# Optimization experiments

Hardware: AMD Instinct MI355X
Metric: run time of the kernel (lower is better)

The kernel has to match this reference:

```python
import jax, jax.numpy as jnp
import numpy as np

N, D_IN, D_H, D_ATT, C_CLUST, N_CLS = 10000, 1024, 512, 256, 10, 4


def setup_inputs() -> dict:
    key = jax.random.key(0)
    ks = jax.random.split(key, 20)
    s = 0.02
    return {
        "x": jax.random.normal(ks[0], (N, D_IN), dtype=jnp.float32),
        "cluster_id": jax.random.randint(ks[1], (N,), 0, C_CLUST, dtype=jnp.int64),
        # per-cluster phi: Linear(1024->512) + ReLU + Linear(512->512) + ReLU
        "W1": s * jax.random.normal(ks[2], (C_CLUST, D_IN, D_H), dtype=jnp.float32),
        "b1": jnp.zeros((C_CLUST, D_H), dtype=jnp.float32),
        "W2": s * jax.random.normal(ks[3], (C_CLUST, D_H, D_H), dtype=jnp.float32),
        "b2": jnp.zeros((C_CLUST, D_H), dtype=jnp.float32),
        # attention_net fc: Linear(512->512)+ReLU
        "Wfc": s * jax.random.normal(ks[4], (D_H, D_H), dtype=jnp.float32),
        "bfc": jnp.zeros((D_H,), dtype=jnp.float32),
        # Attn_Net_Gated
        "Wa": s * jax.random.normal(ks[5], (D_H, D_ATT), dtype=jnp.float32),
        "ba": jnp.zeros((D_ATT,), dtype=jnp.float32),
        "Wb": s * jax.random.normal(ks[6], (D_H, D_ATT), dtype=jnp.float32),
        "bb": jnp.zeros((D_ATT,), dtype=jnp.float32),
        "Wc": s * jax.random.normal(ks[7], (D_ATT, 1), dtype=jnp.float32),
        "bc": jnp.zeros((1,), dtype=jnp.float32),
        # rho: Linear(512->256)+ReLU
        "Wr": s * jax.random.normal(ks[8], (D_H, D_ATT), dtype=jnp.float32),
        "br": jnp.zeros((D_ATT,), dtype=jnp.float32),
        # classifier: Linear(256->4)
        "Wcls": s * jax.random.normal(ks[9], (D_ATT, N_CLS), dtype=jnp.float32),
        "bcls": jnp.zeros((N_CLS,), dtype=jnp.float32),
    }


def reference(x, cluster_id, W1, b1, W2, b2, Wfc, bfc, Wa, ba, Wb, bb, Wc, bc, Wr, br, Wcls, bcls):
    C = W1.shape[0]
    # dense dispatch: apply every cluster's phi, then masked-mean per cluster
    # (ReLU is per-point elementwise, so masked mean == mean over members)
    h1 = jax.nn.relu(jnp.einsum('nd,cdh->cnh', x, W1) + b1[:, None, :])   # [C,N,512]
    h2 = jax.nn.relu(jnp.einsum('cnh,chk->cnk', h1, W2) + b2[:, None, :]) # [C,N,512]
    mask = (cluster_id[None, :] == jnp.arange(C)[:, None]).astype(h2.dtype)  # [C,N]
    counts = jnp.maximum(mask.sum(axis=1), 1.0)                           # [C]
    pooled = jnp.einsum('cnk,cn->ck', h2, mask) / counts[:, None]         # [C,512]
    # attention_net: fc + gated attention
    h = jax.nn.relu(pooled @ Wfc + bfc)                                   # [C,512]
    gate = jnp.tanh(h @ Wa + ba) * jax.nn.sigmoid(h @ Wb + bb)            # [C,256]
    A = (gate @ Wc + bc)                                                  # [C,1]
    A = jax.nn.softmax(A.T, axis=1)                                       # [1,C]
    h_path = A @ h                                                        # [1,512]
    hr = jax.nn.relu(h_path @ Wr + br)                                    # [1,256]
    logits = (hr[0] @ Wcls + bcls)[None, :]                               # [1,4]
    Y_prob = jax.nn.softmax(logits, axis=1)
    Y_hat = jnp.argmax(logits, axis=1)[:, None]
    return logits, Y_prob, Y_hat
```

## Files before the change

### kernel.cpp

```cpp
#include <hip/hip_runtime.h>
#include <math.h>

#define DIN 1024
#define DH 512
#define DATT 256
#define CNUM 10
#define NCLS 4
#define NH 64
#define NSC 40

typedef __attribute__((ext_vector_type(8))) short bf16x8;
typedef __attribute__((ext_vector_type(4))) float f32x4;
typedef unsigned short ushort_t;
typedef unsigned int uint_t;

__device__ inline ushort_t f2bf(float f) {
    uint_t u = __float_as_uint(f);
    u += 0x7FFF + ((u >> 16) & 1);
    return (ushort_t)(u >> 16);
}

__device__ inline void gl_lds16(const void* g, void* l) {
    __builtin_amdgcn_global_load_lds(
        (const __attribute__((address_space(1))) unsigned int*)g,
        (__attribute__((address_space(3))) unsigned int*)l, 16, 0, 0);
}


__global__ __launch_bounds__(256) void k_pre1(
    const float* __restrict__ x, const int* __restrict__ cid, int n,
    const float* __restrict__ bc,
    const float* __restrict__ W1, const float* __restrict__ W2,
    ushort_t* __restrict__ xb, ushort_t* __restrict__ W1t, ushort_t* __restrict__ W2t,
    int nxb, int nw,
    int* __restrict__ counts_part, float* __restrict__ pooled, float* __restrict__ a_logit)
{
    int bid = blockIdx.x;
    int t = threadIdx.x;

    if (bid < nxb) {
        int row = bid * 2 + (t >> 7);
        if (row >= n) return;
        int col = (t & 127) * 8;
        const float* src = x + (size_t)row * DIN + col;
        float4 v0 = *(const float4*)(src);
        float4 v1 = *(const float4*)(src + 4);
        ushort_t* dst = xb + (size_t)row * DIN + col;
        *(ushort4*)dst = make_ushort4(f2bf(v0.x), f2bf(v0.y), f2bf(v0.z), f2bf(v0.w));
        *(ushort4*)(dst + 4) = make_ushort4(f2bf(v1.x), f2bf(v1.y), f2bf(v1.z), f2bf(v1.w));
        return;
    }
    bid -= nxb;

    if (bid < nw) {
        __shared__ float tile[64][65];
        int z = bid >> 7;
        int kx = (bid & 127) >> 3;
        int ny = bid & 7;
        const float* src; ushort_t* dst; int K;
        if (z < CNUM) { K = DIN; src = W1 + (size_t)z * K * DH; dst = W1t + (size_t)z * DH * K; }
        else          { K = DH;  src = W2 + (size_t)(z - CNUM) * K * DH; dst = W2t + (size_t)(z - CNUM) * DH * K; }
        int k0 = kx * 64;
        if (k0 >= K) return;
        int n0 = ny * 64;
        int rr = t >> 4;
        int cc = (t & 15) * 4;
        #pragma unroll
        for (int i = 0; i < 4; i++) {
            int row = rr + 16 * i;
            float4 v = *(const float4*)(src + (size_t)(k0 + row) * DH + n0 + cc);
            tile[row][cc + 0] = v.x; tile[row][cc + 1] = v.y;
            tile[row][cc + 2] = v.z; tile[row][cc + 3] = v.w;
        }
        __syncthreads();
        #pragma unroll
        for (int i = 0; i < 4; i++) {
            int nrow = rr + 16 * i;
            ushort4 o = make_ushort4(f2bf(tile[cc + 0][nrow]), f2bf(tile[cc + 1][nrow]),
                                     f2bf(tile[cc + 2][nrow]), f2bf(tile[cc + 3][nrow]));
            *(ushort4*)(dst + (size_t)(n0 + nrow) * K + k0 + cc) = o;
        }
        return;
    }
    bid -= nw;

    if (bid < NH) {
        __shared__ int h[CNUM];
        int lane = t & 63;
        if (t < CNUM) h[t] = 0;
        __syncthreads();
        for (int i = bid * 256 + t; i < n; i += NH * 256) {
            int c = cid[i];
            #pragma unroll
            for (int cc = 0; cc < CNUM; cc++) {
                unsigned long long mask = __ballot(c == cc);
                if (mask == 0ull) continue;
                if (lane == (__ffsll(mask) - 1)) atomicAdd(&h[cc], __popcll(mask));
            }
        }
        __syncthreads();
        if (t < CNUM) counts_part[bid * 16 + t] = h[t];
        return;
    }

    for (int i = t; i < CNUM * DH; i += 256) pooled[i] = 0.f;
    if (t < CNUM) a_logit[t] = bc[0];
}


__global__ void k_pre2(
    const int* __restrict__ counts_part,
    int* __restrict__ counts, int* __restrict__ offsets, int* __restrict__ tile_off,
    int* __restrict__ cursors)
{
    int t = threadIdx.x;
    if (t < CNUM) {
        int s = 0;
        #pragma unroll 8
        for (int b = 0; b < NH; b++) s += counts_part[b * 16 + t];
        counts[t] = s;
    }
    __syncthreads();
    if (t == 0) {
        int a = 0, tt = 0;
        for (int c = 0; c < CNUM; c++) {
            offsets[c] = a; tile_off[c] = tt; cursors[c] = a;
            a += counts[c]; tt += (counts[c] + 127) >> 7;
        }
        offsets[CNUM] = a; tile_off[CNUM] = tt;
    }
}


__global__ __launch_bounds__(256) void k_pre3(
    const int* __restrict__ cid, int n,
    int* __restrict__ cursors, int* __restrict__ bucket)
{
    int t = threadIdx.x;
    int lane = t & 63;
    for (int i = blockIdx.x * 256 + t; i < n; i += NSC * 256) {
        int c = cid[i];
        #pragma unroll
        for (int cc = 0; cc < CNUM; cc++) {
            unsigned long long mask = __ballot(c == cc);
            if (mask == 0ull) continue;
            int leader = __ffsll(mask) - 1;
            int basep = 0;
            if (lane == leader) basep = atomicAdd(&cursors[cc], __popcll(mask));
            basep = __shfl(basep, leader, 64);
            if (c == cc) {
                int rank = __popcll(mask & ((1ull << lane) - 1ull));
                bucket[basep + rank] = i;
            }
        }
    }
}


__device__ inline void gemm_tile(
    const ushort_t* aSrc0, const ushort_t* aSrc1,
    const ushort_t* bSrc0, const ushort_t* bSrc1, int Kd,
    f32x4 acc[4][4], ushort_t As[128][32], ushort_t Bs[128][32])
{
    int t = threadIdx.x;
    int lane = t & 63;
    int w = t >> 6, wr = w >> 1, wc = w & 1;
    int m = lane & 15, quad = lane >> 4;

    int r0 = t >> 2;
    int kc = (t & 3) * 8;

    ushort_t* aDst0 = &As[r0][kc];
    ushort_t* aDst1 = &As[64 + r0][kc];
    ushort_t* bDst0 = &Bs[r0][kc];
    ushort_t* bDst1 = &Bs[64 + r0][kc];

    const ushort_t* aF = &As[64 * wr + m][quad * 8];
    const ushort_t* bF = &Bs[64 * wc + m][quad * 8];

    for (int k0 = 0; k0 < Kd; k0 += 32) {
        __syncthreads();
        gl_lds16(aSrc0 + k0, aDst0);
        gl_lds16(aSrc1 + k0, aDst1);
        gl_lds16(bSrc0 + k0, bDst0);
        gl_lds16(bSrc1 + k0, bDst1);
        __syncthreads();
        bf16x8 a[4], b[4];
        #pragma unroll
        for (int mf = 0; mf < 4; mf++) a[mf] = *(const bf16x8*)(aF + mf * 16 * 32);
        #pragma unroll
        for (int nf = 0; nf < 4; nf++) b[nf] = *(const bf16x8*)(bF + nf * 16 * 32);
        #pragma unroll
        for (int mf = 0; mf < 4; mf++)
            #pragma unroll
            for (int nf = 0; nf < 4; nf++)
                acc[mf][nf] = __builtin_amdgcn_mfma_f32_16x16x32_bf16(a[mf], b[nf], acc[mf][nf], 0, 0, 0);
    }
}

__global__ __launch_bounds__(256, 1) void k_mfma1(
    const ushort_t* __restrict__ xb, const ushort_t* __restrict__ W1t,
    const float* __restrict__ b1, const int* __restrict__ bucket,
    const int* __restrict__ offsets, const int* __restrict__ counts,
    const int* __restrict__ tile_off,
    ushort_t* __restrict__ H1)
{
    __shared__ ushort_t As[128][32];
    __shared__ ushort_t Bs[128][32];
    int tx = blockIdx.x;
    if (tx >= tile_off[CNUM]) return;
    int c = 0;
    while (tx >= tile_off[c + 1]) c++;
    int m0 = (tx - tile_off[c]) * 128;
    int base = offsets[c], cnt = counts[c];
    int tile_n = blockIdx.y * 128;

    int t = threadIdx.x;
    int r0 = t >> 2;
    int kc = (t & 3) * 8;
    int ra0 = m0 + r0;      if (ra0 > cnt - 1) ra0 = cnt - 1; if (ra0 < 0) ra0 = 0;
    int ra1 = m0 + 64 + r0; if (ra1 > cnt - 1) ra1 = cnt - 1; if (ra1 < 0) ra1 = 0;
    const ushort_t* aSrc0 = xb + (size_t)bucket[base + ra0] * DIN + kc;
    const ushort_t* aSrc1 = xb + (size_t)bucket[base + ra1] * DIN + kc;
    const ushort_t* bSrc0 = W1t + ((size_t)c * DH + tile_n + r0) * DIN + kc;
    const ushort_t* bSrc1 = W1t + ((size_t)c * DH + tile_n + 64 + r0) * DIN + kc;

    f32x4 acc[4][4] = {};
    gemm_tile(aSrc0, aSrc1, bSrc0, bSrc1, DIN, acc, As, Bs);

    int lane = t & 63;
    int w = t >> 6, wr = w >> 1, wc = w & 1;
    int m = lane & 15, quad = lane >> 4;
    int col0 = tile_n + 64 * wc;
    #pragma unroll
    for (int nf = 0; nf < 4; nf++) {
        int col = col0 + 16 * nf + m;
        float bv = b1[c * DH + col];
        #pragma unroll
        for (int mf = 0; mf < 4; mf++) {
            int rowb = m0 + 64 * wr + 16 * mf + quad * 4;
            #pragma unroll
            for (int r = 0; r < 4; r++) {
                int row = rowb + r;
                if (row < cnt)
                    H1[(size_t)(base + row) * DH + col] = f2bf(fmaxf(acc[mf][nf][r] + bv, 0.f));
            }
        }
    }
}

__global__ __launch_bounds__(256, 1) void k_mfma2(
    const ushort_t* __restrict__ H1, const ushort_t* __restrict__ W2t,
    const float* __restrict__ b2,
    const int* __restrict__ offsets, const int* __restrict__ counts,
    const int* __restrict__ tile_off,
    float* __restrict__ pooled)
{
    __shared__ ushort_t As[128][32];
    __shared__ ushort_t Bs[128][32];
    int tx = blockIdx.x;
    if (tx >= tile_off[CNUM]) return;
    int c = 0;
    while (tx >= tile_off[c + 1]) c++;
    int m0 = (tx - tile_off[c]) * 128;
    int base = offsets[c], cnt = counts[c];
    int tile_n = blockIdx.y * 128;

    int t = threadIdx.x;
    int r0 = t >> 2;
    int kc = (t & 3) * 8;
    int ra0 = m0 + r0;      if (ra0 > cnt - 1) ra0 = cnt - 1; if (ra0 < 0) ra0 = 0;
    int ra1 = m0 + 64 + r0; if (ra1 > cnt - 1) ra1 = cnt - 1; if (ra1 < 0) ra1 = 0;
    const ushort_t* aSrc0 = H1 + (size_t)(base + ra0) * DH + kc;
    const ushort_t* aSrc1 = H1 + (size_t)(base + ra1) * DH + kc;
    const ushort_t* bSrc0 = W2t + ((size_t)c * DH + tile_n + r0) * DH + kc;
    const ushort_t* bSrc1 = W2t + ((size_t)c * DH + tile_n + 64 + r0) * DH + kc;

    f32x4 acc[4][4] = {};
    gemm_tile(aSrc0, aSrc1, bSrc0, bSrc1, DH, acc, As, Bs);

    int lane = t & 63;
    int w = t >> 6, wr = w >> 1, wc = w & 1;
    int m = lane & 15, quad = lane >> 4;
    int col0 = tile_n + 64 * wc;
    #pragma unroll
    for (int nf = 0; nf < 4; nf++) {
        int col = col0 + 16 * nf + m;
        float bv = b2[c * DH + col];
        float s = 0.f;
        #pragma unroll
        for (int mf = 0; mf < 4; mf++) {
            int rowb = m0 + 64 * wr + 16 * mf + quad * 4;
            #pragma unroll
            for (int r = 0; r < 4; r++) {
                int row = rowb + r;
                if (row < cnt) s += fmaxf(acc[mf][nf][r] + bv, 0.f);
            }
        }
        s += __shfl_xor(s, 16);
        s += __shfl_xor(s, 32);
        if (quad == 0) atomicAdd(&pooled[c * DH + col], s);
    }
}


#define MT 64
#define NT 128
#define KT 32

__global__ __launch_bounds__(256) void k_gemm1(
    const float* __restrict__ x, const float* __restrict__ W1, const float* __restrict__ b1,
    const int* __restrict__ bucket, const int* __restrict__ offsets, const int* __restrict__ counts,
    float* __restrict__ H1)
{
    int c = blockIdx.z;
    int cnt = counts[c];
    int m0 = blockIdx.x * MT;
    if (m0 >= cnt) return;
    int rows = min(MT, cnt - m0);
    int n0 = blockIdx.y * NT;
    int base = offsets[c];

    __shared__ float As[KT][MT + 4];
    __shared__ float Bs[KT][NT];

    int t = threadIdx.x;
    int tr = t >> 4;
    int tc = t & 15;
    int lr = t >> 2;
    int lk = (t & 3) * 8;
    const float* xrow = nullptr;
    if (lr < rows) xrow = x + (size_t)bucket[base + m0 + lr] * DIN;

    float acc[4][8];
    #pragma unroll
    for (int i = 0; i < 4; i++)
        #pragma unroll
        for (int j = 0; j < 8; j++) acc[i][j] = 0.f;
// ... 108 lines not shown
        #pragma unroll
        for (int k = 0; k < KT; k++) {
            float4 av  = *(const float4*)&As[k][4 * tr];
            float4 bv0 = *(const float4*)&Bs[k][4 * tc];
            float4 bv1 = *(const float4*)&Bs[k][64 + 4 * tc];
            float a[4] = {av.x, av.y, av.z, av.w};
            float b[8] = {bv0.x, bv0.y, bv0.z, bv0.w, bv1.x, bv1.y, bv1.z, bv1.w};
            #pragma unroll
            for (int i = 0; i < 4; i++)
                #pragma unroll
                for (int j = 0; j < 8; j++)
                    acc[i][j] = fmaf(a[i], b[j], acc[i][j]);
        }
    }

    __syncthreads();
    #pragma unroll
    for (int j = 0; j < 8; j++) {
        int cidx = (j < 4) ? (4 * tc + j) : (64 + 4 * tc + (j - 4));
        float bias = b2[c * DH + n0 + cidx];
        float s = 0.f;
        #pragma unroll
        for (int i = 0; i < 4; i++) {
            if (4 * tr + i < rows) s += fmaxf(acc[i][j] + bias, 0.f);
        }
        red[tr][cidx] = s;
    }
    __syncthreads();
    if (t < NT) {
        float s = 0.f;
        #pragma unroll
        for (int r = 0; r < 16; r++) s += red[r][t];
        atomicAdd(&pooled[c * DH + n0 + t], s);
    }
}


__global__ __launch_bounds__(256) void k_fc2(
    const float* __restrict__ pooled, const int* __restrict__ counts,
    const float* __restrict__ Wfc, const float* __restrict__ bfc,
    float* __restrict__ hfc)
{
    int c = blockIdx.x;
    int c0 = blockIdx.y * 64;
    __shared__ float ps[DH];
    __shared__ float red[4][64];
    int t = threadIdx.x;
    float cnt = fmaxf((float)counts[c], 1.f);
    ps[t] = pooled[c * DH + t] / cnt;
    ps[t + 256] = pooled[c * DH + t + 256] / cnt;
    __syncthreads();
    int col = c0 + (t & 63);
    int ks = t >> 6;
    float acc = 0.f;
    #pragma unroll 8
    for (int k = ks * 128; k < ks * 128 + 128; k++)
        acc = fmaf(ps[k], Wfc[(size_t)k * DH + col], acc);
    red[ks][t & 63] = acc;
    __syncthreads();
    if (t < 64) {
        float v = red[0][t] + red[1][t] + red[2][t] + red[3][t] + bfc[c0 + t];
        hfc[c * DH + c0 + t] = fmaxf(v, 0.f);
    }
}

__global__ __launch_bounds__(256) void k_gate2(
    const float* __restrict__ hfc,
    const float* __restrict__ Wa, const float* __restrict__ ba,
    const float* __restrict__ Wb, const float* __restrict__ bb,
    const float* __restrict__ Wc,
    float* __restrict__ a_logit)
{
    int c = blockIdx.x;
    int d0 = blockIdx.y * 64;
    __shared__ float hf[DH];
    __shared__ float ra[4][64], rb[4][64];
    int t = threadIdx.x;
    hf[t] = hfc[c * DH + t];
    hf[t + 256] = hfc[c * DH + t + 256];
    __syncthreads();
    int d = d0 + (t & 63);
    int ks = t >> 6;
    float ga = 0.f, gb = 0.f;
    #pragma unroll 8
    for (int k = ks * 128; k < ks * 128 + 128; k++) {
        float h = hf[k];
        ga = fmaf(h, Wa[(size_t)k * DATT + d], ga);
        gb = fmaf(h, Wb[(size_t)k * DATT + d], gb);
    }
    ra[ks][t & 63] = ga;
    rb[ks][t & 63] = gb;
    __syncthreads();
    if (t < 64) {
        float sa = ra[0][t] + ra[1][t] + ra[2][t] + ra[3][t] + ba[d0 + t];
        float sb = rb[0][t] + rb[1][t] + rb[2][t] + rb[3][t] + bb[d0 + t];
        float g = tanhf(sa) * (1.f / (1.f + expf(-sb)));
        float p = g * Wc[d0 + t];
        #pragma unroll
        for (int off = 32; off >= 1; off >>= 1) p += __shfl_down(p, off, 64);
        if (t == 0) atomicAdd(&a_logit[c], p);
    }
}

__global__ __launch_bounds__(1024) void k_final(
    const float* __restrict__ hfc, const float* __restrict__ a_logit,
    const float* __restrict__ Wr, const float* __restrict__ br,
    const float* __restrict__ Wcls, const float* __restrict__ bcls,
    float* __restrict__ out)
{
    int t = threadIdx.x;
    __shared__ float hp[DH];
    __shared__ float r1[4][DATT];
    __shared__ float hr[DATT];
    __shared__ float wred[4][NCLS];

    float al[CNUM];
    float m = -1e30f;
    #pragma unroll
    for (int c = 0; c < CNUM; c++) { al[c] = a_logit[c]; m = fmaxf(m, al[c]); }
    float s = 0.f;
    #pragma unroll
    for (int c = 0; c < CNUM; c++) { al[c] = expf(al[c] - m); s += al[c]; }
    float inv = 1.f / s;

    if (t < DH) {
        float v = 0.f;
        #pragma unroll
        for (int c = 0; c < CNUM; c++) v = fmaf(al[c] * inv, hfc[c * DH + t], v);
        hp[t] = v;
    }
    __syncthreads();

    int d = t & 255;
    int ks = t >> 8;
    float acc = 0.f;
    #pragma unroll 8
    for (int k = ks * 128; k < ks * 128 + 128; k++)
        acc = fmaf(hp[k], Wr[(size_t)k * DATT + d], acc);
    r1[ks][d] = acc;
    __syncthreads();
    if (t < DATT)
        hr[t] = fmaxf(r1[0][t] + r1[1][t] + r1[2][t] + r1[3][t] + br[t], 0.f);
    __syncthreads();

    if (t < 256) {
        float h = hr[t];
        #pragma unroll
        for (int cls = 0; cls < NCLS; cls++) {
            float p = h * Wcls[(size_t)t * NCLS + cls];
            #pragma unroll
            for (int off = 32; off >= 1; off >>= 1) p += __shfl_down(p, off, 64);
            if ((t & 63) == 0) wred[t >> 6][cls] = p;
        }
    }
    __syncthreads();
    if (t == 0) {
        float lg[NCLS];
        #pragma unroll
        for (int cls = 0; cls < NCLS; cls++)
            lg[cls] = bcls[cls] + wred[0][cls] + wred[1][cls] + wred[2][cls] + wred[3][cls];
        float mm = lg[0];
        #pragma unroll
        for (int i = 1; i < NCLS; i++) mm = fmaxf(mm, lg[i]);
        float ss = 0.f, pr[NCLS];
        #pragma unroll
        for (int i = 0; i < NCLS; i++) { pr[i] = expf(lg[i] - mm); ss += pr[i]; }
        int am = 0; float best = lg[0];
        #pragma unroll
        for (int i = 1; i < NCLS; i++) if (lg[i] > best) { best = lg[i]; am = i; }
        #pragma unroll
        for (int i = 0; i < NCLS; i++) out[i] = lg[i];
        #pragma unroll
        for (int i = 0; i < NCLS; i++) out[4 + i] = pr[i] / ss;
        out[8] = (float)am;
    }
}


extern "C" void kernel_launch(void* const* d_in, const int* in_sizes, int n_in,
                              void* d_out, int out_size, void* d_ws, size_t ws_size,
                              hipStream_t stream) {
    (void)n_in; (void)out_size;
    const float* x    = (const float*)d_in[0];
    const int*   cid  = (const int*)d_in[1];
    const float* W1   = (const float*)d_in[2];
    const float* b1   = (const float*)d_in[3];
    const float* W2   = (const float*)d_in[4];
    const float* b2   = (const float*)d_in[5];
    const float* Wfc  = (const float*)d_in[6];
    const float* bfc  = (const float*)d_in[7];
    const float* Wa   = (const float*)d_in[8];
    const float* ba   = (const float*)d_in[9];
    const float* Wb   = (const float*)d_in[10];
    const float* bb   = (const float*)d_in[11];
    const float* Wc   = (const float*)d_in[12];
    const float* bc   = (const float*)d_in[13];
    const float* Wr   = (const float*)d_in[14];
    const float* br   = (const float*)d_in[15];
    const float* Wcls = (const float*)d_in[16];
    const float* bcls = (const float*)d_in[17];
    float* out = (float*)d_out;
    float* ws  = (float*)d_ws;

    int n = in_sizes[1];

    float* pooled     = ws + 0;
    int*   counts     = (int*)(ws + 5120);
    int*   offsets    = (int*)(ws + 5136);
    int*   tile_off   = (int*)(ws + 5152);
    float* a_logit    = ws + 5168;
    int*   cursors    = (int*)(ws + 5184);
    float* hfc        = ws + 5200;
    int*   counts_part= (int*)(ws + 10320);
    int*   bucket     = (int*)(ws + 11344);

    size_t big0 = (((size_t)(11344 + n) * 4) + 255) & ~(size_t)255;
    size_t w1t_bytes = (size_t)CNUM * DH * DIN * 2;
    size_t w2t_bytes = (size_t)CNUM * DH * DH * 2;
    size_t h1_bytes  = (size_t)n * DH * 2;
    size_t xb_bytes  = (size_t)n * DIN * 2;
    size_t need = big0 + w1t_bytes + w2t_bytes + h1_bytes + xb_bytes;

    ushort_t* W1t = (ushort_t*)((char*)d_ws + big0);
    ushort_t* W2t = (ushort_t*)((char*)d_ws + big0 + w1t_bytes);
    ushort_t* H1  = (ushort_t*)((char*)d_ws + big0 + w1t_bytes + w2t_bytes);
    ushort_t* xb  = (ushort_t*)((char*)d_ws + big0 + w1t_bytes + w2t_bytes + h1_bytes);

    int fast = (ws_size >= need) ? 1 : 0;
    int nxb = fast ? (n + 1) / 2 : 0;
    int nw  = fast ? 128 * 2 * CNUM : 0;
    int pre1_blocks = nxb + nw + NH + 1;

    k_pre1<<<pre1_blocks, 256, 0, stream>>>(
        x, cid, n, bc, W1, W2, xb, W1t, W2t, nxb, nw,
        counts_part, pooled, a_logit);
    k_pre2<<<1, 64, 0, stream>>>(counts_part, counts, offsets, tile_off, cursors);
    k_pre3<<<NSC, 256, 0, stream>>>(cid, n, cursors, bucket);

    if (fast) {
        int maxt = n / 128 + CNUM;
        k_mfma1<<<dim3(maxt, DH / 128), 256, 0, stream>>>(xb, W1t, b1, bucket, offsets, counts, tile_off, H1);
        k_mfma2<<<dim3(maxt, DH / 128), 256, 0, stream>>>(H1, W2t, b2, offsets, counts, tile_off, pooled);
    } else {
        float* H1f = ws + ((11344 + n + 31) & ~31);
        dim3 gg((n + MT - 1) / MT, DH / NT, CNUM);
        k_gemm1<<<gg, 256, 0, stream>>>(x, W1, b1, bucket, offsets, counts, H1f);
        k_gemm2<<<gg, 256, 0, stream>>>(H1f, W2, b2, offsets, counts, pooled);
    }

    k_fc2<<<dim3(CNUM, 8), 256, 0, stream>>>(pooled, counts, Wfc, bfc, hfc);
    k_gate2<<<dim3(CNUM, 4), 256, 0, stream>>>(hfc, Wa, ba, Wb, bb, Wc, a_logit);
    k_final<<<1, 1024, 0, stream>>>(hfc, a_logit, Wr, br, Wcls, bcls, out);
}
```

Measured before the change: 245.4 us.

## Fuse pre2/pre3 into scatter kernel and merge tail kernels with spin-wait flags

Merges the count-prefix kernel into the scatter kernel: every block recomputes the offsets and scatters with per-cluster relative cursors. The three tail kernels (fc, gate, final) become one 121-block launch that orders its phases with atomic done-counters and spin-waits. The GEMM grids are also transposed so blocks that share an M-tile launch next to each other. The aim is to cut launch overhead and improve L2 reuse of the gathered A rows, at the cost of spin-wait deadlock risk if the dependent blocks are not co-resident.

After: 258.4 us. +5.3%, slower.

```diff
diff --git a/kernel.cpp b/kernel.cpp
--- a/kernel.cpp
+++ b/kernel.cpp
@@ -26,6 +26,10 @@
         (__attribute__((address_space(3))) unsigned int*)l, 16, 0, 0);
 }
 
+__device__ inline float agent_load(const float* p) {
+    return __hip_atomic_load(p, __ATOMIC_RELAXED, __HIP_MEMORY_SCOPE_AGENT);
+}
+
 
 __global__ __launch_bounds__(256) void k_pre1(
     const float* __restrict__ x, const int* __restrict__ cid, int n,
@@ -33,7 +37,8 @@
     const float* __restrict__ W1, const float* __restrict__ W2,
     ushort_t* __restrict__ xb, ushort_t* __restrict__ W1t, ushort_t* __restrict__ W2t,
     int nxb, int nw,
-    int* __restrict__ counts_part, float* __restrict__ pooled, float* __restrict__ a_logit)
+    int* __restrict__ counts_part, float* __restrict__ pooled, float* __restrict__ a_logit,
+    int* __restrict__ scat_pos, int* __restrict__ fc_done, int* __restrict__ gate_done)
 {
     int bid = blockIdx.x;
     int t = threadIdx.x;
@@ -105,38 +110,39 @@
 
     for (int i = t; i < CNUM * DH; i += 256) pooled[i] = 0.f;
     if (t < CNUM) a_logit[t] = bc[0];
-}
-
-
-__global__ void k_pre2(
-    const int* __restrict__ counts_part,
+    if (t < CNUM) scat_pos[t] = 0;
+    if (t < CNUM) fc_done[t] = 0;
+    if (t == 0) gate_done[0] = 0;
+}
+
+
+__global__ __launch_bounds__(256) void k_scat(
+    const int* __restrict__ cid, int n, const int* __restrict__ counts_part,
     int* __restrict__ counts, int* __restrict__ offsets, int* __restrict__ tile_off,
-    int* __restrict__ cursors)
+    int* __restrict__ scat_pos, int* __restrict__ bucket)
 {
+    __shared__ int cnts[CNUM], off[CNUM];
     int t = threadIdx.x;
     if (t < CNUM) {
         int s = 0;
         #pragma unroll 8
         for (int b = 0; b < NH; b++) s += counts_part[b * 16 + t];
-        counts[t] = s;
+        cnts[t] = s;
     }
     __syncthreads();
     if (t == 0) {
-        int a = 0, tt = 0;
-        for (int c = 0; c < CNUM; c++) {
-            offsets[c] = a; tile_off[c] = tt; cursors[c] = a;
-            a += counts[c]; tt += (counts[c] + 127) >> 7;
-        }
-        offsets[CNUM] = a; tile_off[CNUM] = tt;
-    }
-}
-
-
-__global__ __launch_bounds__(256) void k_pre3(
-    const int* __restrict__ cid, int n,
-    int* __restrict__ cursors, int* __restrict__ bucket)
-{
-    int t = threadIdx.x;
+        int a = 0;
+        for (int c = 0; c < CNUM; c++) { off[c] = a; a += cnts[c]; }
+        if (blockIdx.x == 0) {
+            int aa = 0, tt = 0;
+            for (int c = 0; c < CNUM; c++) {
+                offsets[c] = aa; tile_off[c] = tt; counts[c] = cnts[c];
+                aa += cnts[c]; tt += (cnts[c] + 127) >> 7;
+            }
+            offsets[CNUM] = aa; tile_off[CNUM] = tt;
+        }
+    }
+    __syncthreads();
     int lane = t & 63;
     for (int i = blockIdx.x * 256 + t; i < n; i += NSC * 256) {
         int c = cid[i];
@@ -146,11 +152,11 @@
             if (mask == 0ull) continue;
             int leader = __ffsll(mask) - 1;
             int basep = 0;
-            if (lane == leader) basep = atomicAdd(&cursors[cc], __popcll(mask));
+            if (lane == leader) basep = atomicAdd(&scat_pos[cc], __popcll(mask));
             basep = __shfl(basep, leader, 64);
             if (c == cc) {
                 int rank = __popcll(mask & ((1ull << lane) - 1ull));
-                bucket[basep + rank] = i;
+                bucket[off[cc] + basep + rank] = i;
             }
         }
     }
@@ -207,13 +213,13 @@
 {
     __shared__ ushort_t As[128][32];
     __shared__ ushort_t Bs[128][32];
-    int tx = blockIdx.x;
+    int tx = blockIdx.y;
     if (tx >= tile_off[CNUM]) return;
     int c = 0;
     while (tx >= tile_off[c + 1]) c++;
     int m0 = (tx - tile_off[c]) * 128;
     int base = offsets[c], cnt = counts[c];
-    int tile_n = blockIdx.y * 128;
+    int tile_n = blockIdx.x * 128;
 
     int t = threadIdx.x;
     int r0 = t >> 2;
@@ -258,13 +264,13 @@
 {
     __shared__ ushort_t As[128][32];
     __shared__ ushort_t Bs[128][32];
-    int tx = blockIdx.x;
+    int tx = blockIdx.y;
     if (tx >= tile_off[CNUM]) return;
     int c = 0;
     while (tx >= tile_off[c + 1]) c++;
     int m0 = (tx - tile_off[c]) * 128;
     int base = offsets[c], cnt = counts[c];
-    int tile_n = blockIdx.y * 128;
+    int tile_n = blockIdx.x * 128;
 
     int t = threadIdx.x;
     int r0 = t >> 2;
@@ -300,6 +306,145 @@
         s += __shfl_xor(s, 16);
         s += __shfl_xor(s, 32);
         if (quad == 0) atomicAdd(&pooled[c * DH + col], s);
+    }
+}
+
+
+__global__ __launch_bounds__(256) void k_tail(
+    const float* __restrict__ pooled, const int* __restrict__ counts,
+    const float* __restrict__ Wfc, const float* __restrict__ bfc,
+    const float* __restrict__ Wa, const float* __restrict__ ba,
+    const float* __restrict__ Wb, const float* __restrict__ bb,
+    const float* __restrict__ Wc,
+    const float* __restrict__ Wr, const float* __restrict__ br,
+    const float* __restrict__ Wcls, const float* __restrict__ bcls,
+    float* __restrict__ hfc, float* __restrict__ a_logit,
+    int* __restrict__ fc_done, int* __restrict__ gate_done,
+    float* __restrict__ out)
+{
+    __shared__ float sh0[DH];
+    __shared__ float red4[4][DATT];
+    __shared__ float hr[DATT];
+    __shared__ float wred[4][NCLS];
+
+    int bid = blockIdx.x, t = threadIdx.x;
+
+    if (bid < 80) {
+        int c = bid >> 3;
+        int c0 = (bid & 7) * 64;
+        float cnt = fmaxf((float)counts[c], 1.f);
+        sh0[t] = pooled[c * DH + t] / cnt;
+        sh0[t + 256] = pooled[c * DH + t + 256] / cnt;
+        __syncthreads();
+        int col = c0 + (t & 63);
+        int ks = t >> 6;
+        float acc = 0.f;
+        #pragma unroll 8
+        for (int k = ks * 128; k < ks * 128 + 128; k++)
+            acc = fmaf(sh0[k], Wfc[(size_t)k * DH + col], acc);
+        red4[ks][t & 63] = acc;
+        __syncthreads();
+        if (t < 64) {
+            float v = red4[0][t] + red4[1][t] + red4[2][t] + red4[3][t] + bfc[c0 + t];
+            hfc[c * DH + c0 + t] = fmaxf(v, 0.f);
+        }
+        __threadfence();
+        __syncthreads();
+        if (t == 0) atomicAdd(&fc_done[c], 1);
+        return;
+    }
+
+    if (bid < 120) {
+        int b = bid - 80;
+        int c = b >> 2;
+        int d0 = (b & 3) * 64;
+        if (t == 0) { while (atomicAdd(&fc_done[c], 0) < 8) {} }
+        __syncthreads();
+        __threadfence();
+        sh0[t] = agent_load(&hfc[c * DH + t]);
+        sh0[t + 256] = agent_load(&hfc[c * DH + t + 256]);
+        __syncthreads();
+        int d = d0 + (t & 63);
+        int ks = t >> 6;
+        float ga = 0.f, gb = 0.f;
+        #pragma unroll 8
+        for (int k = ks * 128; k < ks * 128 + 128; k++) {
+            float h = sh0[k];
+            ga = fmaf(h, Wa[(size_t)k * DATT + d], ga);
+            gb = fmaf(h, Wb[(size_t)k * DATT + d], gb);
+        }
+        red4[ks][t & 63] = ga;
+        red4[ks][(t & 63) + 64] = gb;
+        __syncthreads();
+        if (t < 64) {
+            float sa = red4[0][t] + red4[1][t] + red4[2][t] + red4[3][t] + ba[d0 + t];
+            float sb = red4[0][t + 64] + red4[1][t + 64] + red4[2][t + 64] + red4[3][t + 64] + bb[d0 + t];
+            float g = tanhf(sa) * (1.f / (1.f + expf(-sb)));
+            float p = g * Wc[d0 + t];
+            #pragma unroll
+            for (int off = 32; off >= 1; off >>= 1) p += __shfl_down(p, off, 64);
+            if (t == 0) atomicAdd(&a_logit[c], p);
+        }
+        __threadfence();
+        __syncthreads();
+        if (t == 0) atomicAdd(gate_done, 1);
+        return;
+    }
+
+    if (t == 0) { while (atomicAdd(gate_done, 0) < 40) {} }
+    __syncthreads();
+    __threadfence();
+
+    float al[CNUM];
+    float m = -1e30f;
+    #pragma unroll
+    for (int c = 0; c < CNUM; c++) { al[c] = agent_load(&a_logit[c]); m = fmaxf(m, al[c]); }
+    float s = 0.f;
+    #pragma unroll
+    for (int c = 0; c < CNUM; c++) { al[c] = expf(al[c] - m); s += al[c]; }
+    float inv = 1.f / s;
+
+    for (int kk = t; kk < DH; kk += 256) {
+        float v = 0.f;
+        #pragma unroll
+        for (int c = 0; c < CNUM; c++) v = fmaf(al[c] * inv, agent_load(&hfc[c * DH + kk]), v);
+        sh0[kk] = v;
+    }
+    __syncthreads();
+
+    float acc = br[t];
+    for (int k = 0; k < DH; k++) acc = fmaf(sh0[k], Wr[(size_t)k * DATT + t], acc);
+    hr[t] = fmaxf(acc, 0.f);
+    __syncthreads();
+
+    float h = hr[t];
+    #pragma unroll
+    for (int cls = 0; cls < NCLS; cls++) {
+        float p = h * Wcls[(size_t)t * NCLS + cls];
+        #pragma unroll
+        for (int off = 32; off >= 1; off >>= 1) p += __shfl_down(p, off, 64);
+        if ((t & 63) == 0) wred[t >> 6][cls] = p;
+    }
+    __syncthreads();
+    if (t == 0) {
+        float lg[NCLS];
+        #pragma unroll
+        for (int cls = 0; cls < NCLS; cls++)
+            lg[cls] = bcls[cls] + wred[0][cls] + wred[1][cls] + wred[2][cls] + wred[3][cls];
+        float mm = lg[0];
+        #pragma unroll
+        for (int i = 1; i < NCLS; i++) mm = fmaxf(mm, lg[i]);
+        float ss = 0.f, pr[NCLS];
+        #pragma unroll
+        for (int i = 0; i < NCLS; i++) { pr[i] = expf(lg[i] - mm); ss += pr[i]; }
+        int am = 0; float best = lg[0];
+        #pragma unroll
+        for (int i = 1; i < NCLS; i++) if (lg[i] > best) { best = lg[i]; am = i; }
+        #pragma unroll
+        for (int i = 0; i < NCLS; i++) out[i] = lg[i];
+        #pragma unroll
+        for (int i = 0; i < NCLS; i++) out[4 + i] = pr[i] / ss;
+        out[8] = (float)am;
     }
 }
 
@@ -478,147 +623,6 @@
         #pragma unroll
         for (int r = 0; r < 16; r++) s += red[r][t];
         atomicAdd(&pooled[c * DH + n0 + t], s);
-    }
-}
-
-
-__global__ __launch_bounds__(256) void k_fc2(
-    const float* __restrict__ pooled, const int* __restrict__ counts,
-    const float* __restrict__ Wfc, const float* __restrict__ bfc,
-    float* __restrict__ hfc)
-{
-    int c = blockIdx.x;
-    int c0 = blockIdx.y * 64;
-    __shared__ float ps[DH];
-    __shared__ float red[4][64];
-    int t = threadIdx.x;
-    float cnt = fmaxf((float)counts[c], 1.f);
-    ps[t] = pooled[c * DH + t] / cnt;
-    ps[t + 256] = pooled[c * DH + t + 256] / cnt;
-    __syncthreads();
-    int col = c0 + (t & 63);
-    int ks = t >> 6;
-    float acc = 0.f;
-    #pragma unroll 8
-    for (int k = ks * 128; k < ks * 128 + 128; k++)
-        acc = fmaf(ps[k], Wfc[(size_t)k * DH + col], acc);
-    red[ks][t & 63] = acc;
-    __syncthreads();
-    if (t < 64) {
-        float v = red[0][t] + red[1][t] + red[2][t] + red[3][t] + bfc[c0 + t];
-        hfc[c * DH + c0 + t] = fmaxf(v, 0.f);
-    }
-}
-
-__global__ __launch_bounds__(256) void k_gate2(
-    const float* __restrict__ hfc,
-    const float* __restrict__ Wa, const float* __restrict__ ba,
-    const float* __restrict__ Wb, const float* __restrict__ bb,
-    const float* __restrict__ Wc,
-    float* __restrict__ a_logit)
-{
-    int c = blockIdx.x;
-    int d0 = blockIdx.y * 64;
-    __shared__ float hf[DH];
-    __shared__ float ra[4][64], rb[4][64];
-    int t = threadIdx.x;
-    hf[t] = hfc[c * DH + t];
-    hf[t + 256] = hfc[c * DH + t + 256];
-    __syncthreads();
-    int d = d0 + (t & 63);
-    int ks = t >> 6;
-    float ga = 0.f, gb = 0.f;
-    #pragma unroll 8
-    for (int k = ks * 128; k < ks * 128 + 128; k++) {
-        float h = hf[k];
-        ga = fmaf(h, Wa[(size_t)k * DATT + d], ga);
-        gb = fmaf(h, Wb[(size_t)k * DATT + d], gb);
-    }
-    ra[ks][t & 63] = ga;
-    rb[ks][t & 63] = gb;
-    __syncthreads();
-    if (t < 64) {
-        float sa = ra[0][t] + ra[1][t] + ra[2][t] + ra[3][t] + ba[d0 + t];
-        float sb = rb[0][t] + rb[1][t] + rb[2][t] + rb[3][t] + bb[d0 + t];
-        float g = tanhf(sa) * (1.f / (1.f + expf(-sb)));
-        float p = g * Wc[d0 + t];
-        #pragma unroll
-        for (int off = 32; off >= 1; off >>= 1) p += __shfl_down(p, off, 64);
-        if (t == 0) atomicAdd(&a_logit[c], p);
-    }
-}
-
-__global__ __launch_bounds__(1024) void k_final(
-    const float* __restrict__ hfc, const float* __restrict__ a_logit,
-    const float* __restrict__ Wr, const float* __restrict__ br,
-    const float* __restrict__ Wcls, const float* __restrict__ bcls,
-    float* __restrict__ out)
-{
-    int t = threadIdx.x;
-    __shared__ float hp[DH];
-    __shared__ float r1[4][DATT];
-    __shared__ float hr[DATT];
-    __shared__ float wred[4][NCLS];
-
-    float al[CNUM];
-    float m = -1e30f;
-    #pragma unroll
-    for (int c = 0; c < CNUM; c++) { al[c] = a_logit[c]; m = fmaxf(m, al[c]); }
-    float s = 0.f;
-    #pragma unroll
-    for (int c = 0; c < CNUM; c++) { al[c] = expf(al[c] - m); s += al[c]; }
-    float inv = 1.f / s;
-
-    if (t < DH) {
-        float v = 0.f;
-        #pragma unroll
-        for (int c = 0; c < CNUM; c++) v = fmaf(al[c] * inv, hfc[c * DH + t], v);
-        hp[t] = v;
-    }
-    __syncthreads();
-
-    int d = t & 255;
-    int ks = t >> 8;
-    float acc = 0.f;
-    #pragma unroll 8
-    for (int k = ks * 128; k < ks * 128 + 128; k++)
-        acc = fmaf(hp[k], Wr[(size_t)k * DATT + d], acc);
-    r1[ks][d] = acc;
-    __syncthreads();
-    if (t < DATT)
-        hr[t] = fmaxf(r1[0][t] + r1[1][t] + r1[2][t] + r1[3][t] + br[t], 0.f);
-    __syncthreads();
-
-    if (t < 256) {
-        float h = hr[t];
-        #pragma unroll
-        for (int cls = 0; cls < NCLS; cls++) {
-            float p = h * Wcls[(size_t)t * NCLS + cls];
-            #pragma unroll
-            for (int off = 32; off >= 1; off >>= 1) p += __shfl_down(p, off, 64);
-            if ((t & 63) == 0) wred[t >> 6][cls] = p;
-        }
-    }
-    __syncthreads();
-    if (t == 0) {
-        float lg[NCLS];
-        #pragma unroll
-        for (int cls = 0; cls < NCLS; cls++)
-            lg[cls] = bcls[cls] + wred[0][cls] + wred[1][cls] + wred[2][cls] + wred[3][cls];
-        float mm = lg[0];
-        #pragma unroll
-        for (int i = 1; i < NCLS; i++) mm = fmaxf(mm, lg[i]);
-        float ss = 0.f, pr[NCLS];
-        #pragma unroll
-        for (int i = 0; i < NCLS; i++) { pr[i] = expf(lg[i] - mm); ss += pr[i]; }
-        int am = 0; float best = lg[0];
-        #pragma unroll
-        for (int i = 1; i < NCLS; i++) if (lg[i] > best) { best = lg[i]; am = i; }
-        #pragma unroll
-        for (int i = 0; i < NCLS; i++) out[i] = lg[i];
-        #pragma unroll
-        for (int i = 0; i < NCLS; i++) out[4 + i] = pr[i] / ss;
-        out[8] = (float)am;
     }
 }
 
@@ -655,12 +659,14 @@
     int*   offsets    = (int*)(ws + 5136);
     int*   tile_off   = (int*)(ws + 5152);
     float* a_logit    = ws + 5168;
-    int*   cursors    = (int*)(ws + 5184);
-    float* hfc        = ws + 5200;
-    int*   counts_part= (int*)(ws + 10320);
-    int*   bucket     = (int*)(ws + 11344);
-
-    size_t big0 = (((size_t)(11344 + n) * 4) + 255) & ~(size_t)255;
+    int*   scat_pos   = (int*)(ws + 5184);
+    int*   fc_done    = (int*)(ws + 5200);
+    int*   gate_done  = (int*)(ws + 5216);
+    float* hfc        = ws + 5232;
+    int*   counts_part= (int*)(ws + 10352);
+    int*   bucket     = (int*)(ws + 11376);
+
+    size_t big0 = (((size_t)(11376 + n) * 4) + 255) & ~(size_t)255;
     size_t w1t_bytes = (size_t)CNUM * DH * DIN * 2;
     size_t w2t_bytes = (size_t)CNUM * DH * DH * 2;
     size_t h1_bytes  = (size_t)n * DH * 2;
@@ -679,22 +685,22 @@
 
     k_pre1<<<pre1_blocks, 256, 0, stream>>>(
         x, cid, n, bc, W1, W2, xb, W1t, W2t, nxb, nw,
-        counts_part, pooled, a_logit);
-    k_pre2<<<1, 64, 0, stream>>>(counts_part, counts, offsets, tile_off, cursors);
-    k_pre3<<<NSC, 256, 0, stream>>>(cid, n, cursors, bucket);
+        counts_part, pooled, a_logit, scat_pos, fc_done, gate_done);
+    k_scat<<<NSC, 256, 0, stream>>>(cid, n, counts_part, counts, offsets, tile_off,
+                                    scat_pos, bucket);
 
     if (fast) {
         int maxt = n / 128 + CNUM;
-        k_mfma1<<<dim3(maxt, DH / 128), 256, 0, stream>>>(xb, W1t, b1, bucket, offsets, counts, tile_off, H1);
-        k_mfma2<<<dim3(maxt, DH / 128), 256, 0, stream>>>(H1, W2t, b2, offsets, counts, tile_off, pooled);
+        k_mfma1<<<dim3(4, maxt), 256, 0, stream>>>(xb, W1t, b1, bucket, offsets, counts, tile_off, H1);
+        k_mfma2<<<dim3(4, maxt), 256, 0, stream>>>(H1, W2t, b2, offsets, counts, tile_off, pooled);
     } else {
-        float* H1f = ws + ((11344 + n + 31) & ~31);
+        float* H1f = ws + ((11376 + n + 31) & ~31);
         dim3 gg((n + MT - 1) / MT, DH / NT, CNUM);
         k_gemm1<<<gg, 256, 0, stream>>>(x, W1, b1, bucket, offsets, counts, H1f);
         k_gemm2<<<gg, 256, 0, stream>>>(H1f, W2, b2, offsets, counts, pooled);
     }
 
-    k_fc2<<<dim3(CNUM, 8), 256, 0, stream>>>(pooled, counts, Wfc, bfc, hfc);
-    k_gate2<<<dim3(CNUM, 4), 256, 0, stream>>>(hfc, Wa, ba, Wb, bb, Wc, a_logit);
-    k_final<<<1, 1024, 0, stream>>>(hfc, a_logit, Wr, br, Wcls, bcls, out);
-}
+    k_tail<<<121, 256, 0, stream>>>(pooled, counts, Wfc, bfc, Wa, ba, Wb, bb, Wc,
+                                    Wr, br, Wcls, bcls, hfc, a_logit,
+                                    fc_done, gate_done, out);
+}
```

## Merge preprocessing kernels and swap GEMM grid axes for column-tile adjacency

Applied to the files above, without the earlier changes.

Replaces the three preprocessing launches with two. The histogram runs first, then a single kernel computes prefix offsets per block and scatters bucket indices, alongside the bf16 conversion and weight transposes. This removes one launch and its serialization. The MFMA grids are also transposed so the four column tiles of one row tile are adjacent in launch order, which may improve L2 reuse of gathered A rows. The risk is that every scatter block redundantly reduces counts_part.

Result: faster. 231.3 us, median of 2 (-5.8%).

```diff
diff --git a/kernel.cpp b/kernel.cpp
--- a/kernel.cpp
+++ b/kernel.cpp
@@ -27,16 +27,92 @@
 }
 
 
-__global__ __launch_bounds__(256) void k_pre1(
-    const float* __restrict__ x, const int* __restrict__ cid, int n,
-    const float* __restrict__ bc,
-    const float* __restrict__ W1, const float* __restrict__ W2,
+__global__ __launch_bounds__(256) void k_hist(
+    const int* __restrict__ cid, int n, const float* __restrict__ bc,
+    int* __restrict__ counts_part, float* __restrict__ pooled,
+    float* __restrict__ a_logit, int* __restrict__ scat_pos)
+{
+    int bid = blockIdx.x;
+    int t = threadIdx.x;
+
+    if (bid < NH) {
+        __shared__ int h[CNUM];
+        int lane = t & 63;
+        if (t < CNUM) h[t] = 0;
+        __syncthreads();
+        for (int i = bid * 256 + t; i < n; i += NH * 256) {
+            int c = cid[i];
+            #pragma unroll
+            for (int cc = 0; cc < CNUM; cc++) {
+                unsigned long long mask = __ballot(c == cc);
+                if (mask == 0ull) continue;
+                if (lane == (__ffsll(mask) - 1)) atomicAdd(&h[cc], __popcll(mask));
+            }
+        }
+        __syncthreads();
+        if (t < CNUM) counts_part[bid * 16 + t] = h[t];
+        return;
+    }
+
+    for (int i = t; i < CNUM * DH; i += 256) pooled[i] = 0.f;
+    if (t < CNUM) a_logit[t] = bc[0];
+    if (t < CNUM) scat_pos[t] = 0;
+}
+
+
+__global__ __launch_bounds__(256) void k_scat2(
+    const int* __restrict__ cid, int n, const int* __restrict__ counts_part,
+    const float* __restrict__ x, const float* __restrict__ W1, const float* __restrict__ W2,
     ushort_t* __restrict__ xb, ushort_t* __restrict__ W1t, ushort_t* __restrict__ W2t,
     int nxb, int nw,
-    int* __restrict__ counts_part, float* __restrict__ pooled, float* __restrict__ a_logit)
+    int* __restrict__ counts, int* __restrict__ offsets, int* __restrict__ tile_off,
+    int* __restrict__ scat_pos, int* __restrict__ bucket)
 {
     int bid = blockIdx.x;
     int t = threadIdx.x;
+
+    if (bid < NSC) {
+        __shared__ int cnts[CNUM], off[CNUM];
+        if (t < CNUM) {
+            int s = 0;
+            #pragma unroll 8
+            for (int b = 0; b < NH; b++) s += counts_part[b * 16 + t];
+            cnts[t] = s;
+        }
+        __syncthreads();
+        if (t == 0) {
+            int a = 0;
+            for (int c = 0; c < CNUM; c++) { off[c] = a; a += cnts[c]; }
+            if (bid == 0) {
+                int aa = 0, tt = 0;
+                for (int c = 0; c < CNUM; c++) {
+                    offsets[c] = aa; tile_off[c] = tt; counts[c] = cnts[c];
+                    aa += cnts[c]; tt += (cnts[c] + 127) >> 7;
+                }
+                offsets[CNUM] = aa; tile_off[CNUM] = tt;
+            }
+        }
+        __syncthreads();
+        int lane = t & 63;
+        for (int i = bid * 256 + t; i < n; i += NSC * 256) {
+            int c = cid[i];
+            #pragma unroll
+            for (int cc = 0; cc < CNUM; cc++) {
+                unsigned long long mask = __ballot(c == cc);
+                if (mask == 0ull) continue;
+                int leader = __ffsll(mask) - 1;
+                int basep = 0;
+                if (lane == leader) basep = atomicAdd(&scat_pos[cc], __popcll(mask));
+                basep = __shfl(basep, leader, 64);
+                if (c == cc) {
+                    int rank = __popcll(mask & ((1ull << lane) - 1ull));
+                    bucket[off[cc] + basep + rank] = i;
+                }
+            }
+        }
+        return;
+    }
+    bid -= NSC;
 
     if (bid < nxb) {
         int row = bid * 2 + (t >> 7);
@@ -80,79 +156,6 @@
                                      f2bf(tile[cc + 2][nrow]), f2bf(tile[cc + 3][nrow]));
             *(ushort4*)(dst + (size_t)(n0 + nrow) * K + k0 + cc) = o;
         }
-        return;
-    }
-    bid -= nw;
-
-    if (bid < NH) {
-        __shared__ int h[CNUM];
-        int lane = t & 63;
-        if (t < CNUM) h[t] = 0;
-        __syncthreads();
-        for (int i = bid * 256 + t; i < n; i += NH * 256) {
-            int c = cid[i];
-            #pragma unroll
-            for (int cc = 0; cc < CNUM; cc++) {
-                unsigned long long mask = __ballot(c == cc);
-                if (mask == 0ull) continue;
-                if (lane == (__ffsll(mask) - 1)) atomicAdd(&h[cc], __popcll(mask));
-            }
-        }
-        __syncthreads();
-        if (t < CNUM) counts_part[bid * 16 + t] = h[t];
-        return;
-    }
-
-    for (int i = t; i < CNUM * DH; i += 256) pooled[i] = 0.f;
-    if (t < CNUM) a_logit[t] = bc[0];
-}
-
-
-__global__ void k_pre2(
-    const int* __restrict__ counts_part,
-    int* __restrict__ counts, int* __restrict__ offsets, int* __restrict__ tile_off,
-    int* __restrict__ cursors)
-{
-    int t = threadIdx.x;
-    if (t < CNUM) {
-        int s = 0;
-        #pragma unroll 8
-        for (int b = 0; b < NH; b++) s += counts_part[b * 16 + t];
-        counts[t] = s;
-    }
-    __syncthreads();
-    if (t == 0) {
-        int a = 0, tt = 0;
-        for (int c = 0; c < CNUM; c++) {
-            offsets[c] = a; tile_off[c] = tt; cursors[c] = a;
-            a += counts[c]; tt += (counts[c] + 127) >> 7;
-        }
-        offsets[CNUM] = a; tile_off[CNUM] = tt;
-    }
-}
-
-
-__global__ __launch_bounds__(256) void k_pre3(
-    const int* __restrict__ cid, int n,
-    int* __restrict__ cursors, int* __restrict__ bucket)
-{
-    int t = threadIdx.x;
-    int lane = t & 63;
-    for (int i = blockIdx.x * 256 + t; i < n; i += NSC * 256) {
-        int c = cid[i];
-        #pragma unroll
-        for (int cc = 0; cc < CNUM; cc++) {
-            unsigned long long mask = __ballot(c == cc);
-            if (mask == 0ull) continue;
-            int leader = __ffsll(mask) - 1;
-            int basep = 0;
-            if (lane == leader) basep = atomicAdd(&cursors[cc], __popcll(mask));
-            basep = __shfl(basep, leader, 64);
-            if (c == cc) {
-                int rank = __popcll(mask & ((1ull << lane) - 1ull));
-                bucket[basep + rank] = i;
-            }
-        }
     }
 }
 
@@ -207,13 +210,13 @@
 {
     __shared__ ushort_t As[128][32];
     __shared__ ushort_t Bs[128][32];
-    int tx = blockIdx.x;
+    int tx = blockIdx.y;
     if (tx >= tile_off[CNUM]) return;
     int c = 0;
     while (tx >= tile_off[c + 1]) c++;
     int m0 = (tx - tile_off[c]) * 128;
     int base = offsets[c], cnt = counts[c];
-    int tile_n = blockIdx.y * 128;
+    int tile_n = blockIdx.x * 128;
 
     int t = threadIdx.x;
     int r0 = t >> 2;
@@ -258,13 +261,13 @@
 {
     __shared__ ushort_t As[128][32];
     __shared__ ushort_t Bs[128][32];
-    int tx = blockIdx.x;
+    int tx = blockIdx.y;
     if (tx >= tile_off[CNUM]) return;
     int c = 0;
     while (tx >= tile_off[c + 1]) c++;
     int m0 = (tx - tile_off[c]) * 128;
     int base = offsets[c], cnt = counts[c];
-    int tile_n = blockIdx.y * 128;
+    int tile_n = blockIdx.x * 128;
 
     int t = threadIdx.x;
     int r0 = t >> 2;
@@ -304,6 +307,147 @@
 }
 
 
+__global__ __launch_bounds__(256) void k_fc2(
+    const float* __restrict__ pooled, const int* __restrict__ counts,
+    const float* __restrict__ Wfc, const float* __restrict__ bfc,
+    float* __restrict__ hfc)
+{
+    int c = blockIdx.x;
+    int c0 = blockIdx.y * 64;
+    __shared__ float ps[DH];
+    __shared__ float red[4][64];
+    int t = threadIdx.x;
+    float cnt = fmaxf((float)counts[c], 1.f);
+    ps[t] = pooled[c * DH + t] / cnt;
+    ps[t + 256] = pooled[c * DH + t + 256] / cnt;
+    __syncthreads();
+    int col = c0 + (t & 63);
+    int ks = t >> 6;
+    float acc = 0.f;
+    #pragma unroll 8
+    for (int k = ks * 128; k < ks * 128 + 128; k++)
+        acc = fmaf(ps[k], Wfc[(size_t)k * DH + col], acc);
+    red[ks][t & 63] = acc;
+    __syncthreads();
+    if (t < 64) {
+        float v = red[0][t] + red[1][t] + red[2][t] + red[3][t] + bfc[c0 + t];
+        hfc[c * DH + c0 + t] = fmaxf(v, 0.f);
+    }
+}
+
+__global__ __launch_bounds__(256) void k_gate2(
+    const float* __restrict__ hfc,
+    const float* __restrict__ Wa, const float* __restrict__ ba,
+    const float* __restrict__ Wb, const float* __restrict__ bb,
+    const float* __restrict__ Wc,
+    float* __restrict__ a_logit)
+{
+    int c = blockIdx.x;
+    int d0 = blockIdx.y * 64;
+    __shared__ float hf[DH];
+    __shared__ float ra[4][64], rb[4][64];
+    int t = threadIdx.x;
+    hf[t] = hfc[c * DH + t];
+    hf[t + 256] = hfc[c * DH + t + 256];
+    __syncthreads();
+    int d = d0 + (t & 63);
+    int ks = t >> 6;
+    float ga = 0.f, gb = 0.f;
+    #pragma unroll 8
+    for (int k = ks * 128; k < ks * 128 + 128; k++) {
+        float h = hf[k];
+        ga = fmaf(h, Wa[(size_t)k * DATT + d], ga);
+        gb = fmaf(h, Wb[(size_t)k * DATT + d], gb);
+    }
+    ra[ks][t & 63] = ga;
+    rb[ks][t & 63] = gb;
+    __syncthreads();
+    if (t < 64) {
+        float sa = ra[0][t] + ra[1][t] + ra[2][t] + ra[3][t] + ba[d0 + t];
+        float sb = rb[0][t] + rb[1][t] + rb[2][t] + rb[3][t] + bb[d0 + t];
+        float g = tanhf(sa) * (1.f / (1.f + expf(-sb)));
+        float p = g * Wc[d0 + t];
+        #pragma unroll
+        for (int off = 32; off >= 1; off >>= 1) p += __shfl_down(p, off, 64);
+        if (t == 0) atomicAdd(&a_logit[c], p);
+    }
+}
+
+__global__ __launch_bounds__(1024) void k_final(
+    const float* __restrict__ hfc, const float* __restrict__ a_logit,
+    const float* __restrict__ Wr, const float* __restrict__ br,
+    const float* __restrict__ Wcls, const float* __restrict__ bcls,
+    float* __restrict__ out)
+{
+    int t = threadIdx.x;
+    __shared__ float hp[DH];
+    __shared__ float r1[4][DATT];
+    __shared__ float hr[DATT];
+    __shared__ float wred[4][NCLS];
+
+    float al[CNUM];
+    float m = -1e30f;
+    #pragma unroll
+    for (int c = 0; c < CNUM; c++) { al[c] = a_logit[c]; m = fmaxf(m, al[c]); }
+    float s = 0.f;
+    #pragma unroll
+    for (int c = 0; c < CNUM; c++) { al[c] = expf(al[c] - m); s += al[c]; }
+    float inv = 1.f / s;
+
+    if (t < DH) {
+        float v = 0.f;
+        #pragma unroll
+        for (int c = 0; c < CNUM; c++) v = fmaf(al[c] * inv, hfc[c * DH + t], v);
+        hp[t] = v;
+    }
+    __syncthreads();
+
+    int d = t & 255;
+    int ks = t >> 8;
+    float acc = 0.f;
+    #pragma unroll 8
+    for (int k = ks * 128; k < ks * 128 + 128; k++)
+        acc = fmaf(hp[k], Wr[(size_t)k * DATT + d], acc);
+    r1[ks][d] = acc;
+    __syncthreads();
+    if (t < DATT)
+        hr[t] = fmaxf(r1[0][t] + r1[1][t] + r1[2][t] + r1[3][t] + br[t], 0.f);
+    __syncthreads();
+
+    if (t < 256) {
+        float h = hr[t];
+        #pragma unroll
+        for (int cls = 0; cls < NCLS; cls++) {
+            float p = h * Wcls[(size_t)t * NCLS + cls];
+            #pragma unroll
+            for (int off = 32; off >= 1; off >>= 1) p += __shfl_down(p, off, 64);
+            if ((t & 63) == 0) wred[t >> 6][cls] = p;
+        }
+    }
+    __syncthreads();
+    if (t == 0) {
+        float lg[NCLS];
+        #pragma unroll
+        for (int cls = 0; cls < NCLS; cls++)
+            lg[cls] = bcls[cls] + wred[0][cls] + wred[1][cls] + wred[2][cls] + wred[3][cls];
+        float mm = lg[0];
+        #pragma unroll
+        for (int i = 1; i < NCLS; i++) mm = fmaxf(mm, lg[i]);
+        float ss = 0.f, pr[NCLS];
+        #pragma unroll
+        for (int i = 0; i < NCLS; i++) { pr[i] = expf(lg[i] - mm); ss += pr[i]; }
+        int am = 0; float best = lg[0];
+        #pragma unroll
+        for (int i = 1; i < NCLS; i++) if (lg[i] > best) { best = lg[i]; am = i; }
+        #pragma unroll
+        for (int i = 0; i < NCLS; i++) out[i] = lg[i];
+        #pragma unroll
+        for (int i = 0; i < NCLS; i++) out[4 + i] = pr[i] / ss;
+        out[8] = (float)am;
+    }
+}
+
+
 #define MT 64
 #define NT 128
 #define KT 32
@@ -478,147 +622,6 @@
         #pragma unroll
         for (int r = 0; r < 16; r++) s += red[r][t];
         atomicAdd(&pooled[c * DH + n0 + t], s);
-    }
-}
-
-
-__global__ __launch_bounds__(256) void k_fc2(
-    const float* __restrict__ pooled, const int* __restrict__ counts,
-    const float* __restrict__ Wfc, const float* __restrict__ bfc,
-    float* __restrict__ hfc)
-{
-    int c = blockIdx.x;
-    int c0 = blockIdx.y * 64;
-    __shared__ float ps[DH];
-    __shared__ float red[4][64];
-    int t = threadIdx.x;
-    float cnt = fmaxf((float)counts[c], 1.f);
-    ps[t] = pooled[c * DH + t] / cnt;
-    ps[t + 256] = pooled[c * DH + t + 256] / cnt;
-    __syncthreads();
-    int col = c0 + (t & 63);
-    int ks = t >> 6;
-    float acc = 0.f;
-    #pragma unroll 8
-    for (int k = ks * 128; k < ks * 128 + 128; k++)
-        acc = fmaf(ps[k], Wfc[(size_t)k * DH + col], acc);
-    red[ks][t & 63] = acc;
-    __syncthreads();
-    if (t < 64) {
-        float v = red[0][t] + red[1][t] + red[2][t] + red[3][t] + bfc[c0 + t];
-        hfc[c * DH + c0 + t] = fmaxf(v, 0.f);
-    }
-}
-
-__global__ __launch_bounds__(256) void k_gate2(
-    const float* __restrict__ hfc,
-    const float* __restrict__ Wa, const float* __restrict__ ba,
-    const float* __restrict__ Wb, const float* __restrict__ bb,
-    const float* __restrict__ Wc,
-    float* __restrict__ a_logit)
-{
-    int c = blockIdx.x;
-    int d0 = blockIdx.y * 64;
-    __shared__ float hf[DH];
-    __shared__ float ra[4][64], rb[4][64];
-    int t = threadIdx.x;
-    hf[t] = hfc[c * DH + t];
-    hf[t + 256] = hfc[c * DH + t + 256];
-    __syncthreads();
-    int d = d0 + (t & 63);
-    int ks = t >> 6;
-    float ga = 0.f, gb = 0.f;
-    #pragma unroll 8
-    for (int k = ks * 128; k < ks * 128 + 128; k++) {
-        float h = hf[k];
-        ga = fmaf(h, Wa[(size_t)k * DATT + d], ga);
-        gb = fmaf(h, Wb[(size_t)k * DATT + d], gb);
-    }
-    ra[ks][t & 63] = ga;
-    rb[ks][t & 63] = gb;
-    __syncthreads();
-    if (t < 64) {
-        float sa = ra[0][t] + ra[1][t] + ra[2][t] + ra[3][t] + ba[d0 + t];
-        float sb = rb[0][t] + rb[1][t] + rb[2][t] + rb[3][t] + bb[d0 + t];
-        float g = tanhf(sa) * (1.f / (1.f + expf(-sb)));
-        float p = g * Wc[d0 + t];
-        #pragma unroll
-        for (int off = 32; off >= 1; off >>= 1) p += __shfl_down(p, off, 64);
-        if (t == 0) atomicAdd(&a_logit[c], p);
-    }
-}
-
-__global__ __launch_bounds__(1024) void k_final(
-    const float* __restrict__ hfc, const float* __restrict__ a_logit,
-    const float* __restrict__ Wr, const float* __restrict__ br,
-    const float* __restrict__ Wcls, const float* __restrict__ bcls,
-    float* __restrict__ out)
-{
-    int t = threadIdx.x;
-    __shared__ float hp[DH];
-    __shared__ float r1[4][DATT];
-    __shared__ float hr[DATT];
-    __shared__ float wred[4][NCLS];
-
-    float al[CNUM];
-    float m = -1e30f;
-    #pragma unroll
-    for (int c = 0; c < CNUM; c++) { al[c] = a_logit[c]; m = fmaxf(m, al[c]); }
-    float s = 0.f;
-    #pragma unroll
-    for (int c = 0; c < CNUM; c++) { al[c] = expf(al[c] - m); s += al[c]; }
-    float inv = 1.f / s;
-
-    if (t < DH) {
-        float v = 0.f;
-        #pragma unroll
-        for (int c = 0; c < CNUM; c++) v = fmaf(al[c] * inv, hfc[c * DH + t], v);
-        hp[t] = v;
-    }
-    __syncthreads();
-
-    int d = t & 255;
-    int ks = t >> 8;
-    float acc = 0.f;
-    #pragma unroll 8
-    for (int k = ks * 128; k < ks * 128 + 128; k++)
-        acc = fmaf(hp[k], Wr[(size_t)k * DATT + d], acc);
-    r1[ks][d] = acc;
-    __syncthreads();
-    if (t < DATT)
-        hr[t] = fmaxf(r1[0][t] + r1[1][t] + r1[2][t] + r1[3][t] + br[t], 0.f);
-    __syncthreads();
-
-    if (t < 256) {
-        float h = hr[t];
-        #pragma unroll
-        for (int cls = 0; cls < NCLS; cls++) {
-            float p = h * Wcls[(size_t)t * NCLS + cls];
-            #pragma unroll
-            for (int off = 32; off >= 1; off >>= 1) p += __shfl_down(p, off, 64);
-            if ((t & 63) == 0) wred[t >> 6][cls] = p;
-        }
-    }
-    __syncthreads();
-    if (t == 0) {
-        float lg[NCLS];
-        #pragma unroll
-        for (int cls = 0; cls < NCLS; cls++)
-            lg[cls] = bcls[cls] + wred[0][cls] + wred[1][cls] + wred[2][cls] + wred[3][cls];
-        float mm = lg[0];
-        #pragma unroll
-        for (int i = 1; i < NCLS; i++) mm = fmaxf(mm, lg[i]);
-        float ss = 0.f, pr[NCLS];
-        #pragma unroll
-        for (int i = 0; i < NCLS; i++) { pr[i] = expf(lg[i] - mm); ss += pr[i]; }
-        int am = 0; float best = lg[0];
-        #pragma unroll
-        for (int i = 1; i < NCLS; i++) if (lg[i] > best) { best = lg[i]; am = i; }
-        #pragma unroll
-        for (int i = 0; i < NCLS; i++) out[i] = lg[i];
-        #pragma unroll
-        for (int i = 0; i < NCLS; i++) out[4 + i] = pr[i] / ss;
-        out[8] = (float)am;
     }
 }
 
@@ -655,7 +658,7 @@
     int*   offsets    = (int*)(ws + 5136);
     int*   tile_off   = (int*)(ws + 5152);
     float* a_logit    = ws + 5168;
-    int*   cursors    = (int*)(ws + 5184);
+    int*   scat_pos   = (int*)(ws + 5184);
     float* hfc        = ws + 5200;
     int*   counts_part= (int*)(ws + 10320);
     int*   bucket     = (int*)(ws + 11344);
@@ -675,18 +678,16 @@
     int fast = (ws_size >= need) ? 1 : 0;
     int nxb = fast ? (n + 1) / 2 : 0;
     int nw  = fast ? 128 * 2 * CNUM : 0;
-    int pre1_blocks = nxb + nw + NH + 1;
-
-    k_pre1<<<pre1_blocks, 256, 0, stream>>>(
-        x, cid, n, bc, W1, W2, xb, W1t, W2t, nxb, nw,
-        counts_part, pooled, a_logit);
-    k_pre2<<<1, 64, 0, stream>>>(counts_part, counts, offsets, tile_off, cursors);
-    k_pre3<<<NSC, 256, 0, stream>>>(cid, n, cursors, bucket);
+
+    k_hist<<<NH + 1, 256, 0, stream>>>(cid, n, bc, counts_part, pooled, a_logit, scat_pos);
+    k_scat2<<<NSC + nxb + nw, 256, 0, stream>>>(
+        cid, n, counts_part, x, W1, W2, xb, W1t, W2t, nxb, nw,
+        counts, offsets, tile_off, scat_pos, bucket);
 
     if (fast) {
         int maxt = n / 128 + CNUM;
-        k_mfma1<<<dim3(maxt, DH / 128), 256, 0, stream>>>(xb, W1t, b1, bucket, offsets, counts, tile_off, H1);
-        k_mfma2<<<dim3(maxt, DH / 128), 256, 0, stream>>>(H1, W2t, b2, offsets, counts, tile_off, pooled);
+        k_mfma1<<<dim3(4, maxt), 256, 0, stream>>>(xb, W1t, b1, bucket, offsets, counts, tile_off, H1);
+        k_mfma2<<<dim3(4, maxt), 256, 0, stream>>>(H1, W2t, b2, offsets, counts, tile_off, pooled);
     } else {
         float* H1f = ws + ((11344 + n + 31) & ~31);
         dim3 gg((n + MT - 1) / MT, DH / NT, CNUM);
```
